# Kernel optimization log

Measured on AMD Instinct MI355X. Metric: run time of the kernel, lower is better.

## Reference

```python
import jax, jax.numpy as jnp
import numpy as np

NUM_HEADS = 16

def setup_inputs() -> dict:
    key = jax.random.key(0)
    ks = jax.random.split(key, 5)
    B, T, C = 2, 2048, 1024
    s = 0.02
    return {
        "x": jax.random.normal(ks[0], (B, T, C), dtype=jnp.float32),
        "attn_w": jax.random.normal(ks[1], (3 * C, C), dtype=jnp.float32) * s,
        "attn_b": jax.random.normal(ks[2], (3 * C,), dtype=jnp.float32) * s,
        "proj_w": jax.random.normal(ks[3], (C, C), dtype=jnp.float32) * s,
        "proj_b": jax.random.normal(ks[4], (C,), dtype=jnp.float32) * s,
    }

def reference(x, attn_w, attn_b, proj_w, proj_b):
    B, T, C = x.shape
    H = NUM_HEADS
    D = C // H
    # fused QKV projection (torch Linear: x @ W^T + b)
    qkv = x @ attn_w.T + attn_b                      # [B, T, 3C]
    q, k, v = jnp.split(qkv, 3, axis=-1)             # each [B, T, C]
    # split heads -> [B, H, T, D]
    def heads(t):
        return t.reshape(B, T, H, D).transpose(0, 2, 1, 3)
    q, k, v = heads(q), heads(k), heads(v)
    scale = 1.0 / jnp.sqrt(jnp.asarray(D, dtype=x.dtype))
    scores = jnp.einsum("bhtd,bhsd->bhts", q, k) * scale   # [B, H, T, T]
    causal = jnp.tril(jnp.ones((T, T), dtype=bool))
    scores = jnp.where(causal[None, None], scores, jnp.asarray(-jnp.inf, dtype=scores.dtype))
    att = jax.nn.softmax(scores, axis=-1)
    out = jnp.einsum("bhts,bhsd->bhtd", att, v)      # [B, H, T, D]
    out = out.transpose(0, 2, 1, 3).reshape(B, T, C)
    return out @ proj_w.T + proj_b
```

## Files before the change

kernel.cpp:

```cpp
#include <hip/hip_runtime.h>
#include <hip/hip_bf16.h>

typedef __bf16 bf16_t;
typedef __bf16 bf16x4 __attribute__((ext_vector_type(4)));
typedef __bf16 bf16x8 __attribute__((ext_vector_type(8)));
typedef float f32x4 __attribute__((ext_vector_type(4)));
typedef float f32x8 __attribute__((ext_vector_type(8)));

#define MFMA16(a, b, c) __builtin_amdgcn_mfma_f32_16x16x32_bf16(a, b, c, 0, 0, 0)

#define GLOAD_LDS16(g, l)                                              \
  __builtin_amdgcn_global_load_lds(                                    \
      (const __attribute__((address_space(1))) unsigned int*)(g),      \
      (__attribute__((address_space(3))) unsigned int*)(l), 16, 0, 0)

constexpr int B = 2, T = 2048, C = 1024, H = 16, D = 64;
constexpr int NQKV = 3 * C;
constexpr int M = B * T;

#define QSCALE 0.18033688011112042f

__global__ __launch_bounds__(256) void cvt_kernel(
    const float* __restrict__ s0, bf16_t* __restrict__ d0, int n0,
    const float* __restrict__ s1, bf16_t* __restrict__ d1, int n1,
    const float* __restrict__ s2, bf16_t* __restrict__ d2, int n2)
{
  const float* s; bf16_t* d; int n;
  if (blockIdx.y == 0)      { s = s0; d = d0; n = n0; }
  else if (blockIdx.y == 1) { s = s1; d = d1; n = n1; }
  else                      { s = s2; d = d2; n = n2; }
  const int idx = (blockIdx.x * 256 + threadIdx.x) * 8;
  if (idx >= n) return;
  f32x8 t = *(const f32x8*)(s + idx);
  bf16x8 r;
#pragma unroll
  for (int j = 0; j < 8; ++j) r[j] = (bf16_t)t[j];
  *(bf16x8*)(d + idx) = r;
}

template<int BM, int BN, int MI, int NI>
__device__ __forceinline__ void gemm_mainloop_db(
    const bf16_t* __restrict__ A, const bf16_t* __restrict__ Wt,
    const int K, const int m0, const int n0,
    bf16_t* ldsA0, bf16_t* ldsA1, bf16_t* ldsB0, bf16_t* ldsB1,
    f32x4 acc[MI][NI])
{
  const int tid  = threadIdx.x;
  const int wv   = tid >> 6;
  const int lane = tid & 63;
  const int col  = lane & 15;
  const int quad = lane >> 4;
  const int lr8  = lane >> 3;
  const int cpos = lane & 7;
  const int wm = wv >> 1, wn = wv & 1;
  constexpr int AJ = BM / 32;
  constexpr int ARW = BM / 4;
  constexpr int BJ = BN / 32;
  constexpr int BRW = BN / 4;

  const bf16_t* ag[AJ]; const bf16_t* bg[BJ];
#pragma unroll
  for (int j = 0; j < AJ; ++j)
    ag[j] = A + (size_t)(m0 + wv * ARW + j * 8 + lr8) * K + (cpos ^ lr8) * 8;
#pragma unroll
  for (int j = 0; j < BJ; ++j)
    bg[j] = Wt + (size_t)(n0 + wv * BRW + j * 8 + lr8) * K + (cpos ^ lr8) * 8;

  const int xa = quad ^ (col & 7);
  const int niter = K / 64;

#pragma unroll
  for (int j = 0; j < AJ; ++j)
    GLOAD_LDS16(ag[j], ldsA0 + (wv * ARW + j * 8) * 64);
#pragma unroll
  for (int j = 0; j < BJ; ++j)
    GLOAD_LDS16(bg[j], ldsB0 + (wv * BRW + j * 8) * 64);

  for (int it = 0; it < niter; ++it) {
    __syncthreads();
    const bf16_t* cA = (it & 1) ? ldsA1 : ldsA0;
    const bf16_t* cB = (it & 1) ? ldsB1 : ldsB0;
    if (it + 1 < niter) {
      bf16_t* nA = (it & 1) ? ldsA0 : ldsA1;
      bf16_t* nB = (it & 1) ? ldsB0 : ldsB1;
      const int off = (it + 1) * 64;
#pragma unroll
      for (int j = 0; j < AJ; ++j)
        GLOAD_LDS16(ag[j] + off, nA + (wv * ARW + j * 8) * 64);
#pragma unroll
      for (int j = 0; j < BJ; ++j)
        GLOAD_LDS16(bg[j] + off, nB + (wv * BRW + j * 8) * 64);
    }
#pragma unroll
    for (int ks = 0; ks < 2; ++ks) {
      const int xk = (xa ^ (ks * 4)) * 8;
      bf16x8 af[MI], bfr[NI];
#pragma unroll
      for (int mi = 0; mi < MI; ++mi)
        af[mi] = *(const bf16x8*)(cA + (wm * (MI * 16) + mi * 16 + col) * 64 + xk);
#pragma unroll
      for (int ni = 0; ni < NI; ++ni)
        bfr[ni] = *(const bf16x8*)(cB + (wn * (NI * 16) + ni * 16 + col) * 64 + xk);
#pragma unroll
      for (int mi = 0; mi < MI; ++mi)
#pragma unroll
        for (int ni = 0; ni < NI; ++ni)
          acc[mi][ni] = MFMA16(af[mi], bfr[ni], acc[mi][ni]);
    }
  }
}

__global__ __launch_bounds__(256) void qkv_gemm_kernel(
    const bf16_t* __restrict__ x, const bf16_t* __restrict__ w,
    const float* __restrict__ bias,
    bf16_t* __restrict__ qws, bf16_t* __restrict__ kws, bf16_t* __restrict__ vws)
{
  __shared__ __align__(16) bf16_t ldsA[2][128 * 64];
  __shared__ __align__(16) bf16_t ldsB[2][128 * 64];
  const int lane = threadIdx.x & 63;
  const int wv   = threadIdx.x >> 6;
  const int col  = lane & 15;
  const int quad = lane >> 4;
  const int wm = wv >> 1, wn = wv & 1;
  const int m0 = blockIdx.y * 128;
  const int n0 = blockIdx.x * 128;

  f32x4 acc[4][4] = {};
  gemm_mainloop_db<128, 128, 4, 4>(x, w, C, m0, n0,
                                   ldsA[0], ldsA[1], ldsB[0], ldsB[1], acc);

  const int which = n0 >> 10;

  if (which == 2) {
    __syncthreads();
    bf16_t* vt = &ldsA[0][0] + wv * 4096;

#pragma unroll
    for (int ni = 0; ni < 4; ++ni) {
      const int n = n0 + wn * 64 + ni * 16 + col;
      const float bval = bias[n];
      const int dl = ni * 16 + col;
#pragma unroll
      for (int r = 0; r < 4; ++r) {
        bf16x4 pw;
#pragma unroll
        for (int mi = 0; mi < 4; ++mi)
          pw[mi] = (bf16_t)(acc[mi][ni][r] + bval);
        const int k = 2 * quad + (r >> 1);
        const int S = dl * 8 + (k ^ (dl & 7));
        *(bf16x4*)(vt + S * 8 + (r & 1) * 4) = pw;
      }
    }

    const int b   = (m0 + wm * 64) >> 11;
    const int t0w = (m0 + wm * 64) & (T - 1);
    const int h   = ((n0 + wn * 64) & (C - 1)) >> 6;
    const size_t bh = (size_t)(b * H + h);
    const int lr8 = lane >> 3;
    const int c8  = lane & 7;
#pragma unroll
    for (int j = 0; j < 8; ++j) {
      const int dl = j * 8 + lr8;
      const int d  = dl;
      bf16x8 row = *(const bf16x8*)(vt + (dl * 8 + (c8 ^ (dl & 7))) * 8);
      *(bf16x8*)(vws + (bh * D + d) * T + t0w + c8 * 8) = row;
    }
  } else {
#pragma unroll
    for (int ni = 0; ni < 4; ++ni) {
      const int n = n0 + wn * 64 + ni * 16 + col;
      const float bval = bias[n];
      const int c = n & (C - 1);
      const int h = c >> 6;
      const int d = c & 63;
#pragma unroll
      for (int mi = 0; mi < 4; ++mi) {
#pragma unroll
        for (int r = 0; r < 4; ++r) {
          const int m = m0 + wm * 64 + mi * 16 + quad * 4 + r;
          const int b = m >> 11;
          const int t = m & (T - 1);
          const size_t bh = (size_t)(b * H + h);
          if (which == 0)
            qws[(bh * T + t) * D + d] = (bf16_t)((acc[mi][ni][r] + bval) * QSCALE);
          else
            kws[(bh * T + t) * D + d] = (bf16_t)(acc[mi][ni][r] + bval);
        }
      }
    }
  }
}

__global__ __launch_bounds__(256) void attn_kernel(
    const bf16_t* __restrict__ qws, const bf16_t* __restrict__ kws,
    const bf16_t* __restrict__ vws, bf16_t* __restrict__ yws)
{
  const int id = blockIdx.x;
  const int bh = id & 31;
  const int pr = id >> 5;
  const int tid  = threadIdx.x;
  const int wv   = tid >> 6;
  const int lane = tid & 63;
  const int col  = lane & 15;
  const int quad = lane >> 4;

  const bf16_t* Q  = qws + (size_t)bh * T * D;
  const bf16_t* K  = kws + (size_t)bh * T * D;
  const bf16_t* Vt = vws + (size_t)bh * D * T;

  __shared__ __align__(16) bf16_t ldsK[2][64 * 64];
  __shared__ __align__(16) bf16_t ldsV[2][64 * 64];
  __shared__ __align__(16) bf16_t ldsPh_s[4][16 * 64];
  __shared__ __align__(16) bf16_t ldsPl_s[4][16 * 64];
  bf16_t* ldsPh = ldsPh_s[wv];
  bf16_t* ldsPl = ldsPl_s[wv];

  const int xs   = col & 7;
  const int cxq  = (quad ^ xs) * 8;
  const int lr8  = lane >> 3;
  const int ksrc = (lane & 7) ^ lr8;
  const int pxor = (quad & 1) * 4;
  const int b = bh >> 4;
  const int h = bh & 15;

  const int qt_h = 31 - pr, qt_l = pr;
  const int t0h = qt_h * 64, t0l = qt_l * 64;
  const int twh = t0h + 16 * wv, twl = t0l + 16 * wv;

  bf16x8 qfh0 = *(const bf16x8*)(Q + (size_t)(twh + col) * D + quad * 8);
  bf16x8 qfh1 = *(const bf16x8*)(Q + (size_t)(twh + col) * D + 32 + quad * 8);
  bf16x8 qfl0 = *(const bf16x8*)(Q + (size_t)(twl + col) * D + quad * 8);
  bf16x8 qfl1 = *(const bf16x8*)(Q + (size_t)(twl + col) * D + 32 + quad * 8);

  f32x4 oh[4] = {}, ol[4] = {};
  f32x4 lph = {}, lpl = {};

  auto stage = [&](int it) {
    const int sn = it * 64;
    bf16_t* dK = ldsK[it & 1];
    bf16_t* dV = ldsV[it & 1];
#pragma unroll
    for (int j = 0; j < 2; ++j) {
      GLOAD_LDS16(K + (size_t)(sn + 16 * wv + j * 8 + lr8) * D + ksrc * 8,
                  dK + (16 * wv + j * 8) * 64);
      GLOAD_LDS16(Vt + (size_t)(16 * wv + j * 8 + lr8) * T + sn + ksrc * 8,
                  dV + (16 * wv + j * 8) * 64);
    }
  };

  auto compute_tile = [&](const bf16_t* bK, const bf16_t* bV, int s0, int tw,
                          bf16x8 qf0, bf16x8 qf1,
                          f32x4 (&o)[4], f32x4& lp, bf16_t* Pw, bool diag) {
    f32x4 sc[4];
    __builtin_amdgcn_s_setprio(1);
#pragma unroll
    for (int kb = 0; kb < 4; ++kb) {
      const bf16_t* kr = bK + (kb * 16 + col) * 64;
      bf16x8 kf0 = *(const bf16x8*)(kr + cxq);
      bf16x8 kf1 = *(const bf16x8*)(kr + (cxq ^ 32));
      f32x4 a = {};
      a = MFMA16(qf0, kf0, a);
      a = MFMA16(qf1, kf1, a);
      sc[kb] = a;
    }
    __builtin_amdgcn_s_setprio(0);
#pragma unroll
    for (int r = 0; r < 4; ++r) {
      const int prow = (quad * 4 + r) * 64;
      const int pxr  = pxor + r;
      bf16x4 pw;
#pragma unroll
      for (int kb = 0; kb < 4; ++kb) {
        float p = __builtin_amdgcn_exp2f(sc[kb][r]);
        if (diag && (s0 + kb * 16 + col > tw + quad * 4 + r)) p = 0.0f;
        lp[r] += p;
        pw[kb] = (bf16_t)p;
      }
      *(bf16x4*)(Pw + prow + (((col >> 1) ^ pxr) * 8) + (col & 1) * 4) = pw;
    }
    __builtin_amdgcn_s_setprio(1);
#pragma unroll
    for (int ks = 0; ks < 2; ++ks) {
      const int xk = cxq ^ (ks * 32);
      bf16x8 pa = *(const bf16x8*)(Pw + col * 64 + xk);
#pragma unroll
      for (int ni = 0; ni < 4; ++ni) {
        bf16x8 vf = *(const bf16x8*)(bV + (ni * 16 + col) * 64 + xk);
        o[ni] = MFMA16(pa, vf, o[ni]);
      }
    }
    __builtin_amdgcn_s_setprio(0);
  };

  stage(0);

  for (int it = 0; it < qt_l; ++it) {
    __syncthreads();
    stage(it + 1);
    const bf16_t* bK = ldsK[it & 1];
    const bf16_t* bV = ldsV[it & 1];
    compute_tile(bK, bV, it * 64, twh, qfh0, qfh1, oh, lph, ldsPh, false);
    compute_tile(bK, bV, it * 64, twl, qfl0, qfl1, ol, lpl, ldsPl, false);
  }
  {
    const int it = qt_l;
    __syncthreads();
    stage(it + 1);
    const bf16_t* bK = ldsK[it & 1];
    const bf16_t* bV = ldsV[it & 1];
    compute_tile(bK, bV, it * 64, twh, qfh0, qfh1, oh, lph, ldsPh, false);
    compute_tile(bK, bV, it * 64, twl, qfl0, qfl1, ol, lpl, ldsPl, true);
  }
  for (int it = qt_l + 1; it < qt_h; ++it) {
    __syncthreads();
    stage(it + 1);
    const bf16_t* bK = ldsK[it & 1];
    const bf16_t* bV = ldsV[it & 1];
    compute_tile(bK, bV, it * 64, twh, qfh0, qfh1, oh, lph, ldsPh, false);
  }
  {
    const int it = qt_h;
    __syncthreads();
    const bf16_t* bK = ldsK[it & 1];
    const bf16_t* bV = ldsV[it & 1];
    compute_tile(bK, bV, it * 64, twh, qfh0, qfh1, oh, lph, ldsPh, true);
  }

#pragma unroll
  for (int r = 0; r < 4; ++r) {
    float l0 = lph[r], l1 = lpl[r];
#pragma unroll
    for (int off = 1; off < 16; off <<= 1) {
      l0 += __shfl_xor(l0, off);
      l1 += __shfl_xor(l1, off);
    }
    const float rl0 = 1.0f / l0, rl1 = 1.0f / l1;
    const int th = twh + quad * 4 + r;
    const int tl = twl + quad * 4 + r;
#pragma unroll
    for (int ni = 0; ni < 4; ++ni) {
      const int d = ni * 16 + col;
      yws[((size_t)(b * T + th)) * C + h * D + d] = (bf16_t)(oh[ni][r] * rl0);
      yws[((size_t)(b * T + tl)) * C + h * D + d] = (bf16_t)(ol[ni][r] * rl1);
    }
  }
}

__global__ __launch_bounds__(256) void proj_gemm_kernel(
    const bf16_t* __restrict__ y, const bf16_t* __restrict__ w,
    const float* __restrict__ bias, float* __restrict__ out)
{
  __shared__ __align__(16) bf16_t ldsA[2][128 * 64];
  __shared__ __align__(16) bf16_t ldsB[2][64 * 64];
  const int lane = threadIdx.x & 63;
  const int wv   = threadIdx.x >> 6;
  const int col  = lane & 15;
  const int quad = lane >> 4;
  const int wm = wv >> 1, wn = wv & 1;
  const int m0 = blockIdx.y * 128;
  const int n0 = blockIdx.x * 64;

  f32x4 acc[4][2] = {};
  gemm_mainloop_db<128, 64, 4, 2>(y, w, C, m0, n0,
                                  ldsA[0], ldsA[1], ldsB[0], ldsB[1], acc);

#pragma unroll
  for (int ni = 0; ni < 2; ++ni) {
    const int n = n0 + wn * 32 + ni * 16 + col;
    const float bval = bias[n];
#pragma unroll
    for (int mi = 0; mi < 4; ++mi) {
#pragma unroll
      for (int r = 0; r < 4; ++r) {
        const int m = m0 + wm * 64 + mi * 16 + quad * 4 + r;
        out[(size_t)m * C + n] = acc[mi][ni][r] + bval;
      }
    }
  }
}

extern "C" void kernel_launch(void* const* d_in, const int* in_sizes, int n_in,
                              void* d_out, int out_size, void* d_ws, size_t ws_size,
                              hipStream_t stream) {
  const float* x      = (const float*)d_in[0];
  const float* attn_w = (const float*)d_in[1];
  const float* attn_b = (const float*)d_in[2];
  const float* proj_w = (const float*)d_in[3];
  const float* proj_b = (const float*)d_in[4];
  float* out = (float*)d_out;

  const size_t E = (size_t)B * H * T * D;
  char* ws = (char*)d_ws;
  bf16_t* qws = (bf16_t*)(ws);
  bf16_t* kws = (bf16_t*)(ws + 2 * E);
  bf16_t* vws = (bf16_t*)(ws + 4 * E);
  bf16_t* yws = (bf16_t*)(ws + 6 * E);
  bf16_t* xb  = (bf16_t*)(ws + 8 * E);
  bf16_t* awb = (bf16_t*)(ws + 10 * E);
  bf16_t* pwb = (bf16_t*)(ws + 11 * E + E / 2);

  const int NX = M * C, NAW = NQKV * C, NPW = C * C;
  cvt_kernel<<<dim3(NX / 2048, 3), 256, 0, stream>>>(
      x, xb, NX, attn_w, awb, NAW, proj_w, pwb, NPW);
  qkv_gemm_kernel<<<dim3(NQKV / 128, M / 128), 256, 0, stream>>>(
      xb, awb, attn_b, qws, kws, vws);
  attn_kernel<<<512, 256, 0, stream>>>(qws, kws, vws, yws);
  proj_gemm_kernel<<<dim3(C / 64, M / 128), 256, 0, stream>>>(
      yws, pwb, proj_b, out);
}
```

Measured before the change: 170.1 us.

## Replace paired causal query tiles with one query tile per block

The attention kernel used to give each block two query tiles, a long one and a short one, so that causal work was balanced and each K/V stage was reused for both. Now each block handles a single query tile, and the grid doubles to 1024 blocks launched heaviest-first. This cuts registers and LDS per block, which can raise occupancy. In exchange, K/V tiles are loaded about twice as often overall and per-block work is uneven, so the scheduler has to absorb the imbalance.

Result: no change. 169.0 us (-0.7%).

```diff
diff --git a/kernel.cpp b/kernel.cpp
--- a/kernel.cpp
+++ b/kernel.cpp
@@ -197,7 +197,7 @@
 {
   const int id = blockIdx.x;
   const int bh = id & 31;
-  const int pr = id >> 5;
+  const int qt = 31 - (id >> 5);
   const int tid  = threadIdx.x;
   const int wv   = tid >> 6;
   const int lane = tid & 63;
@@ -210,10 +210,8 @@
 
   __shared__ __align__(16) bf16_t ldsK[2][64 * 64];
   __shared__ __align__(16) bf16_t ldsV[2][64 * 64];
-  __shared__ __align__(16) bf16_t ldsPh_s[4][16 * 64];
-  __shared__ __align__(16) bf16_t ldsPl_s[4][16 * 64];
-  bf16_t* ldsPh = ldsPh_s[wv];
-  bf16_t* ldsPl = ldsPl_s[wv];
+  __shared__ __align__(16) bf16_t ldsP_s[4][16 * 64];
+  bf16_t* ldsPw = ldsP_s[wv];
 
   const int xs   = col & 7;
   const int cxq  = (quad ^ xs) * 8;
@@ -223,17 +221,14 @@
   const int b = bh >> 4;
   const int h = bh & 15;
 
-  const int qt_h = 31 - pr, qt_l = pr;
-  const int t0h = qt_h * 64, t0l = qt_l * 64;
-  const int twh = t0h + 16 * wv, twl = t0l + 16 * wv;
-
-  bf16x8 qfh0 = *(const bf16x8*)(Q + (size_t)(twh + col) * D + quad * 8);
-  bf16x8 qfh1 = *(const bf16x8*)(Q + (size_t)(twh + col) * D + 32 + quad * 8);
-  bf16x8 qfl0 = *(const bf16x8*)(Q + (size_t)(twl + col) * D + quad * 8);
-  bf16x8 qfl1 = *(const bf16x8*)(Q + (size_t)(twl + col) * D + 32 + quad * 8);
-
-  f32x4 oh[4] = {}, ol[4] = {};
-  f32x4 lph = {}, lpl = {};
+  const int t0 = qt * 64;
+  const int tw = t0 + 16 * wv;
+
+  bf16x8 qf0 = *(const bf16x8*)(Q + (size_t)(tw + col) * D + quad * 8);
+  bf16x8 qf1 = *(const bf16x8*)(Q + (size_t)(tw + col) * D + 32 + quad * 8);
+
+  f32x4 o[4] = {};
+  f32x4 lp = {};
 
   auto stage = [&](int it) {
     const int sn = it * 64;
@@ -248,9 +243,8 @@
     }
   };
 
-  auto compute_tile = [&](const bf16_t* bK, const bf16_t* bV, int s0, int tw,
-                          bf16x8 qf0, bf16x8 qf1,
-                          f32x4 (&o)[4], f32x4& lp, bf16_t* Pw, bool diag) {
+  auto compute_tile = [&](const bf16_t* bK, const bf16_t* bV, int s0,
+                          bool diag) {
     f32x4 sc[4];
     __builtin_amdgcn_s_setprio(1);
 #pragma unroll
@@ -276,13 +270,13 @@
         lp[r] += p;
         pw[kb] = (bf16_t)p;
       }
-      *(bf16x4*)(Pw + prow + (((col >> 1) ^ pxr) * 8) + (col & 1) * 4) = pw;
+      *(bf16x4*)(ldsPw + prow + (((col >> 1) ^ pxr) * 8) + (col & 1) * 4) = pw;
     }
     __builtin_amdgcn_s_setprio(1);
 #pragma unroll
     for (int ks = 0; ks < 2; ++ks) {
       const int xk = cxq ^ (ks * 32);
-      bf16x8 pa = *(const bf16x8*)(Pw + col * 64 + xk);
+      bf16x8 pa = *(const bf16x8*)(ldsPw + col * 64 + xk);
 #pragma unroll
       for (int ni = 0; ni < 4; ++ni) {
         bf16x8 vf = *(const bf16x8*)(bV + (ni * 16 + col) * 64 + xk);
@@ -294,54 +288,28 @@
 
   stage(0);
 
-  for (int it = 0; it < qt_l; ++it) {
+  for (int it = 0; it < qt; ++it) {
     __syncthreads();
     stage(it + 1);
-    const bf16_t* bK = ldsK[it & 1];
-    const bf16_t* bV = ldsV[it & 1];
-    compute_tile(bK, bV, it * 64, twh, qfh0, qfh1, oh, lph, ldsPh, false);
-    compute_tile(bK, bV, it * 64, twl, qfl0, qfl1, ol, lpl, ldsPl, false);
+    compute_tile(ldsK[it & 1], ldsV[it & 1], it * 64, false);
   }
   {
-    const int it = qt_l;
     __syncthreads();
-    stage(it + 1);
-    const bf16_t* bK = ldsK[it & 1];
-    const bf16_t* bV = ldsV[it & 1];
-    compute_tile(bK, bV, it * 64, twh, qfh0, qfh1, oh, lph, ldsPh, false);
-    compute_tile(bK, bV, it * 64, twl, qfl0, qfl1, ol, lpl, ldsPl, true);
-  }
-  for (int it = qt_l + 1; it < qt_h; ++it) {
-    __syncthreads();
-    stage(it + 1);
-    const bf16_t* bK = ldsK[it & 1];
-    const bf16_t* bV = ldsV[it & 1];
-    compute_tile(bK, bV, it * 64, twh, qfh0, qfh1, oh, lph, ldsPh, false);
-  }
-  {
-    const int it = qt_h;
-    __syncthreads();
-    const bf16_t* bK = ldsK[it & 1];
-    const bf16_t* bV = ldsV[it & 1];
-    compute_tile(bK, bV, it * 64, twh, qfh0, qfh1, oh, lph, ldsPh, true);
+    compute_tile(ldsK[qt & 1], ldsV[qt & 1], qt * 64, true);
   }
 
 #pragma unroll
   for (int r = 0; r < 4; ++r) {
-    float l0 = lph[r], l1 = lpl[r];
-#pragma unroll
-    for (int off = 1; off < 16; off <<= 1) {
+    float l0 = lp[r];
+#pragma unroll
+    for (int off = 1; off < 16; off <<= 1)
       l0 += __shfl_xor(l0, off);
-      l1 += __shfl_xor(l1, off);
-    }
-    const float rl0 = 1.0f / l0, rl1 = 1.0f / l1;
-    const int th = twh + quad * 4 + r;
-    const int tl = twl + quad * 4 + r;
+    const float rl0 = 1.0f / l0;
+    const int th = tw + quad * 4 + r;
 #pragma unroll
     for (int ni = 0; ni < 4; ++ni) {
       const int d = ni * 16 + col;
-      yws[((size_t)(b * T + th)) * C + h * D + d] = (bf16_t)(oh[ni][r] * rl0);
-      yws[((size_t)(b * T + tl)) * C + h * D + d] = (bf16_t)(ol[ni][r] * rl1);
+      yws[((size_t)(b * T + th)) * C + h * D + d] = (bf16_t)(o[ni][r] * rl0);
     }
   }
 }
@@ -404,7 +372,7 @@
       x, xb, NX, attn_w, awb, NAW, proj_w, pwb, NPW);
   qkv_gemm_kernel<<<dim3(NQKV / 128, M / 128), 256, 0, stream>>>(
       xb, awb, attn_b, qws, kws, vws);
-  attn_kernel<<<512, 256, 0, stream>>>(qws, kws, vws, yws);
+  attn_kernel<<<1024, 256, 0, stream>>>(qws, kws, vws, yws);
   proj_gemm_kernel<<<dim3(C / 64, M / 128), 256, 0, stream>>>(
       yws, pwb, proj_b, out);
 }
```
